# Kernel optimization log

Measured on AMD Instinct MI355X. Metric: run time of the kernel, lower is better.

Reference implementation:

```python
import jax, jax.numpy as jnp
import numpy as np

B, S, D, H = 2, 2048, 1024, 16
HD = D // H
FF = 4 * D
EPS = 1e-5


def _layernorm(x, g, b):
    m = jnp.mean(x, axis=-1, keepdims=True)
    v = jnp.var(x, axis=-1, keepdims=True)
    return (x - m) * jax.lax.rsqrt(v + EPS) * g + b


def setup_inputs() -> dict:
    key = jax.random.key(0)
    ks = jax.random.split(key, 13)
    s = lambda fan_in: 1.0 / np.sqrt(fan_in)
    return {
        "x": jax.random.normal(ks[0], (B, S, D), jnp.float32),
        "ln1_g": jnp.ones((D,), jnp.float32),
        "ln1_b": jnp.zeros((D,), jnp.float32),
        "w_qkv": jax.random.uniform(ks[1], (D, 3 * D), jnp.float32, -s(D), s(D)),
        "b_qkv": jax.random.uniform(ks[2], (3 * D,), jnp.float32, -s(D), s(D)),
        "w_proj": jax.random.uniform(ks[3], (D, D), jnp.float32, -s(D), s(D)),
        "b_proj": jax.random.uniform(ks[4], (D,), jnp.float32, -s(D), s(D)),
        "ln2_g": jnp.ones((D,), jnp.float32),
        "ln2_b": jnp.zeros((D,), jnp.float32),
        "w_fc1": jax.random.uniform(ks[5], (D, FF), jnp.float32, -s(D), s(D)),
        "b_fc1": jax.random.uniform(ks[6], (FF,), jnp.float32, -s(D), s(D)),
        "w_fc2": jax.random.uniform(ks[7], (FF, D), jnp.float32, -s(FF), s(FF)),
        "b_fc2": jax.random.uniform(ks[8], (D,), jnp.float32, -s(FF), s(FF)),
    }


def reference(x, ln1_g, ln1_b, w_qkv, b_qkv, w_proj, b_proj,
              ln2_g, ln2_b, w_fc1, b_fc1, w_fc2, b_fc2):
    scale = 1.0 / np.sqrt(HD)
    # pre-LN attention
    h = _layernorm(x, ln1_g, ln1_b)
    qkv = h @ w_qkv + b_qkv                                # [B,S,3D]
    qkv = qkv.reshape(B, S, 3, H, HD).transpose(2, 0, 3, 1, 4)
    q, k, v = qkv[0], qkv[1], qkv[2]                       # [B,H,S,HD]
    scores = jnp.einsum("bhqd,bhkd->bhqk", q, k) * scale   # [B,H,S,S]
    causal = jnp.tril(jnp.ones((S, S), bool))
    scores = jnp.where(causal, scores, -jnp.inf)
    attn = jax.nn.softmax(scores, axis=-1)
    out = jnp.einsum("bhqk,bhkd->bhqd", attn, v)           # [B,H,S,HD]
    out = out.transpose(0, 2, 1, 3).reshape(B, S, D)
    out = out @ w_proj + b_proj
    x = x + out
    # pre-LN MLP
    h = _layernorm(x, ln2_g, ln2_b)
    h = jax.nn.gelu(h @ w_fc1 + b_fc1, approximate=False)
    h = h @ w_fc2 + b_fc2
    return x + h
```

## Files before the change

### kernel.cpp

```cpp
#include <hip/hip_runtime.h>
#include <hip/hip_bf16.h>

#define BDIM 1024
#define SEQ  2048
#define NB   2
#define NH   16
#define HDIM 64
#define FFDIM 4096
#define MROWS (NB*SEQ)

typedef __attribute__((ext_vector_type(8))) short short8;
typedef __attribute__((ext_vector_type(4))) float f32x4;

static __device__ __forceinline__ unsigned short f2bf(float f) {
  union { float f; unsigned u; } v; v.f = f;
  unsigned r = v.u + 0x7fffu + ((v.u >> 16) & 1u);
  return (unsigned short)(r >> 16);
}

static __device__ __forceinline__ f32x4 splat4(float x) {
  f32x4 v; v[0] = x; v[1] = x; v[2] = x; v[3] = x; return v;
}

#define GLOAD16(gp, lp)                                                        \
  __builtin_amdgcn_global_load_lds(                                            \
      (const __attribute__((address_space(1))) void*)(gp),                     \
      (__attribute__((address_space(3))) void*)(lp), 16, 0, 0)

__global__ void tcvt_all(const float* __restrict__ w0, const float* __restrict__ w1,
                         const float* __restrict__ w2, const float* __restrict__ w3,
                         unsigned short* __restrict__ o0, unsigned short* __restrict__ o1,
                         unsigned short* __restrict__ o2, unsigned short* __restrict__ o3) {
  const int bid = blockIdx.x;
  const float* in; unsigned short* out; int R, C, nbx, rem;
  if (bid < 3072)      { in = w0; out = o0; R = 1024; C = 3072; rem = bid;        nbx = 96;  }
  else if (bid < 4096) { in = w1; out = o1; R = 1024; C = 1024; rem = bid - 3072; nbx = 32;  }
  else if (bid < 8192) { in = w2; out = o2; R = 1024; C = 4096; rem = bid - 4096; nbx = 128; }
  else                 { in = w3; out = o3; R = 4096; C = 1024; rem = bid - 8192; nbx = 32;  }
  const int c0 = (rem % nbx) * 32, r0 = (rem / nbx) * 32;
  __shared__ float tile[32][33];
  const int tx = threadIdx.x & 31, ty = threadIdx.x >> 5;
#pragma unroll
  for (int i = 0; i < 32; i += 8)
    tile[ty + i][tx] = in[(size_t)(r0 + ty + i) * C + c0 + tx];
  __syncthreads();
#pragma unroll
  for (int i = 0; i < 32; i += 8)
    out[(size_t)(c0 + ty + i) * R + r0 + tx] = f2bf(tile[tx][ty + i]);
}

__global__ void vtr_kernel(const unsigned short* __restrict__ qkv,
                           unsigned short* __restrict__ vt) {
  __shared__ unsigned short tile[32][33];
  const int h = blockIdx.z & 15, b = blockIdx.z >> 4;
  const int s0 = blockIdx.y * 32, d0 = blockIdx.x * 32;
  const int tx = threadIdx.x & 31, ty = threadIdx.x >> 5;
  const unsigned short* src = qkv + (size_t)b * SEQ * 3072 + 2048 + h * HDIM;
#pragma unroll
  for (int i = 0; i < 32; i += 8)
    tile[ty + i][tx] = src[(size_t)(s0 + ty + i) * 3072 + d0 + tx];
  __syncthreads();
  unsigned short* dst = vt + (size_t)(b * NH + h) * HDIM * SEQ;
#pragma unroll
  for (int i = 0; i < 32; i += 8)
    dst[(size_t)(d0 + ty + i) * SEQ + s0 + tx] = tile[tx][ty + i];
}

__global__ void ln_kernel(const float* __restrict__ x, const float* __restrict__ g,
                          const float* __restrict__ b, unsigned short* __restrict__ out) {
  const int row = blockIdx.x;
  const int tid = threadIdx.x;
  const float4 v = ((const float4*)(x + (size_t)row * BDIM))[tid];
  float s  = v.x + v.y + v.z + v.w;
  float ss = v.x * v.x + v.y * v.y + v.z * v.z + v.w * v.w;
#pragma unroll
  for (int off = 32; off; off >>= 1) { s += __shfl_xor(s, off); ss += __shfl_xor(ss, off); }
  __shared__ float red[8];
  const int wave = tid >> 6;
  if ((tid & 63) == 0) { red[wave * 2] = s; red[wave * 2 + 1] = ss; }
  __syncthreads();
  s  = red[0] + red[2] + red[4] + red[6];
  ss = red[1] + red[3] + red[5] + red[7];
  const float mean = s * (1.0f / BDIM);
  const float inv  = rsqrtf(ss * (1.0f / BDIM) - mean * mean + 1e-5f);
  const float4 gg = ((const float4*)g)[tid];
  const float4 bb = ((const float4*)b)[tid];
  ushort4 o;
  o.x = f2bf((v.x - mean) * inv * gg.x + bb.x);
  o.y = f2bf((v.y - mean) * inv * gg.y + bb.y);
  o.z = f2bf((v.z - mean) * inv * gg.z + bb.z);
  o.w = f2bf((v.w - mean) * inv * gg.w + bb.w);
  ((ushort4*)(out + (size_t)row * BDIM))[tid] = o;
}

template <int EPI>
__global__ __launch_bounds__(256, 2)
void gemm_bt(const unsigned short* __restrict__ A, const unsigned short* __restrict__ Bt,
             const float* __restrict__ bias, const float* __restrict__ resid,
             void* __restrict__ outp, int M, int N, int K) {
  __shared__ unsigned short As[128 * 32];
  __shared__ unsigned short Bs[128 * 32];
  const int tid = threadIdx.x;
  const int n0 = blockIdx.x * 128, m0 = blockIdx.y * 128;
  const int lane = tid & 63, wave = tid >> 6;
  const int lr = lane & 15, lg = lane >> 4;
  const int wr = (wave >> 1) * 64, wc = (wave & 1) * 64;

  const unsigned short* ga0 = A  + (size_t)(m0 + (tid >> 2)) * K + (tid & 3) * 8;
  const unsigned short* ga1 = ga0 + (size_t)64 * K;
  const unsigned short* gb0 = Bt + (size_t)(n0 + (tid >> 2)) * K + (tid & 3) * 8;
  const unsigned short* gb1 = gb0 + (size_t)64 * K;
  unsigned short* la0 = As + tid * 8;
  unsigned short* la1 = As + (256 + tid) * 8;
  unsigned short* lb0 = Bs + tid * 8;
  unsigned short* lb1 = Bs + (256 + tid) * 8;

  f32x4 acc[4][4];
#pragma unroll
  for (int i = 0; i < 4; i++)
#pragma unroll
    for (int j = 0; j < 4; j++) acc[i][j] = splat4(0.0f);

  for (int k0 = 0; k0 < K; k0 += 32) {
    GLOAD16(ga0 + k0, la0);
    GLOAD16(ga1 + k0, la1);
    GLOAD16(gb0 + k0, lb0);
    GLOAD16(gb1 + k0, lb1);
    __syncthreads();
    short8 af[4], bfr[4];
#pragma unroll
    for (int mi = 0; mi < 4; mi++)
      af[mi] = *(const short8*)(As + (wr + mi * 16 + lr) * 32 + lg * 8);
#pragma unroll
    for (int ni = 0; ni < 4; ni++)
      bfr[ni] = *(const short8*)(Bs + (wc + ni * 16 + lr) * 32 + lg * 8);
#pragma unroll
    for (int mi = 0; mi < 4; mi++)
#pragma unroll
      for (int ni = 0; ni < 4; ni++)
        acc[mi][ni] = __builtin_amdgcn_mfma_f32_16x16x32_bf16(af[mi], bfr[ni], acc[mi][ni], 0, 0, 0);
    __syncthreads();
  }

  float bv[4];
#pragma unroll
  for (int ni = 0; ni < 4; ni++) bv[ni] = bias[n0 + wc + ni * 16 + lr];
#pragma unroll
  for (int mi = 0; mi < 4; mi++) {
#pragma unroll
    for (int ni = 0; ni < 4; ni++) {
      const int row0 = m0 + wr + mi * 16 + lg * 4;
      const int col  = n0 + wc + ni * 16 + lr;
#pragma unroll
      for (int r = 0; r < 4; r++) {
        const float v = acc[mi][ni][r] + bv[ni];
        const size_t idx = (size_t)(row0 + r) * N + col;
        if constexpr (EPI == 0) {
          ((unsigned short*)outp)[idx] = f2bf(v);
        } else if constexpr (EPI == 1) {
          ((float*)outp)[idx] = v + resid[idx];
        } else {
          const float t = 0.5f * v * (1.0f + erff(v * 0.70710678118f));
          ((unsigned short*)outp)[idx] = f2bf(t);
        }
      }
    }
  }
}

__global__ __launch_bounds__(256, 3)
void attn_kernel(const unsigned short* __restrict__ qkv,
                 const unsigned short* __restrict__ vT,
                 unsigned short* __restrict__ out) {
  __shared__ unsigned short Ks[64 * 64];
  __shared__ unsigned short Vs[64 * 64];
  __shared__ unsigned short Ps[4][32 * 72];
  const int tid = threadIdx.x;
  const int wave = tid >> 6, lane = tid & 63;
  const int lr = lane & 15, lg = lane >> 4;
  const int Q0 = blockIdx.x * 128;
  const int wq0 = Q0 + wave * 32;
  const int h = blockIdx.y, bb = blockIdx.z;
  const size_t base = (size_t)bb * SEQ * 3072;
  const unsigned short* vth = vT + (size_t)(bb * NH + h) * HDIM * SEQ;
  unsigned short* psw = Ps[wave];
  const int sw = lr & 7;

  short8 qf[2][2];
#pragma unroll
  for (int qb = 0; qb < 2; ++qb)
#pragma unroll
    for (int kc = 0; kc < 2; ++kc)
      qf[qb][kc] = *(const short8*)(qkv + base +
          (size_t)(wq0 + qb * 16 + lr) * 3072 + h * HDIM + kc * 32 + lg * 8);

  f32x4 oacc[2][4];
#pragma unroll
  for (int qb = 0; qb < 2; ++qb)
#pragma unroll
    for (int n = 0; n < 4; ++n) oacc[qb][n] = splat4(0.0f);
  f32x4 m_i[2] = { splat4(-INFINITY), splat4(-INFINITY) };
  f32x4 l_i[2] = { splat4(0.0f), splat4(0.0f) };

  const int srow = tid >> 3;
  const int scb  = (tid & 7) ^ (srow & 7);
  const unsigned short* kg0 = qkv + base + (size_t)srow * 3072 + 1024 + h * HDIM + scb * 8;
  const unsigned short* vg0 = vth + (size_t)srow * SEQ + scb * 8;
  unsigned short* kl0 = Ks + tid * 8;
  unsigned short* kl1 = Ks + 2048 + tid * 8;
  unsigned short* vl0 = Vs + tid * 8;
  unsigned short* vl1 = Vs + 2048 + tid * 8;

  const int TB = Q0 / 64 + 2;

  for (int t = 0; t < TB; ++t) {
    const int kk = t * 64;
    __syncthreads();
    GLOAD16(kg0 + (size_t)kk * 3072, kl0);
    GLOAD16(kg0 + (size_t)(kk + 32) * 3072, kl1);
    GLOAD16(vg0 + kk, vl0);
    GLOAD16(vg0 + (size_t)32 * SEQ + kk, vl1);
    __syncthreads();

    short8 kf[4][2];
#pragma unroll
    for (int kb = 0; kb < 4; ++kb)
#pragma unroll
      for (int kc = 0; kc < 2; ++kc)
        kf[kb][kc] = *(const short8*)(Ks + (kb * 16 + lr) * 64 +
                                      (((kc * 4 + lg) ^ sw) * 8));
    f32x4 s[2][4];
#pragma unroll
    for (int qb = 0; qb < 2; ++qb)
#pragma unroll
      for (int kb = 0; kb < 4; ++kb) s[qb][kb] = splat4(0.0f);
    __builtin_amdgcn_s_setprio(1);
#pragma unroll
    for (int qb = 0; qb < 2; ++qb)
#pragma unroll
      for (int kb = 0; kb < 4; ++kb) {
        s[qb][kb] = __builtin_amdgcn_mfma_f32_16x16x32_bf16(qf[qb][0], kf[kb][0], s[qb][kb], 0, 0, 0);
        s[qb][kb] = __builtin_amdgcn_mfma_f32_16x16x32_bf16(qf[qb][1], kf[kb][1], s[qb][kb], 0, 0, 0);
      }
    __builtin_amdgcn_s_setprio(0);

    const bool nm = (kk + 64 > wq0);
#pragma unroll
    for (int qb = 0; qb < 2; ++qb)
#pragma unroll
      for (int kb = 0; kb < 4; ++kb)
#pragma unroll
        for (int r = 0; r < 4; ++r) {
          float v = s[qb][kb][r] * 0.125f;
          if (nm) {
            const int q = wq0 + qb * 16 + lg * 4 + r;
            if (kk + kb * 16 + lr > q) v = -INFINITY;
          }
          s[qb][kb][r] = v;
        }

    f32x4 mx[2];
#pragma unroll
    for (int qb = 0; qb < 2; ++qb) {
#pragma unroll
      for (int r = 0; r < 4; ++r)
        mx[qb][r] = fmaxf(fmaxf(s[qb][0][r], s[qb][1][r]),
                          fmaxf(s[qb][2][r], s[qb][3][r]));
    }
#pragma unroll
    for (int msk = 1; msk < 16; msk <<= 1)
#pragma unroll
      for (int qb = 0; qb < 2; ++qb)
#pragma unroll
        for (int r = 0; r < 4; ++r)
          mx[qb][r] = fmaxf(mx[qb][r], __shfl_xor(mx[qb][r], msk));
    f32x4 mnew[2], corr[2];
#pragma unroll
    for (int qb = 0; qb < 2; ++qb)
#pragma unroll
      for (int r = 0; r < 4; ++r) {
        mnew[qb][r] = fmaxf(m_i[qb][r], mx[qb][r]);
        corr[qb][r] = __expf(m_i[qb][r] - mnew[qb][r]);
      }
#pragma unroll
    for (int qb = 0; qb < 2; ++qb)
#pragma unroll
      for (int kb = 0; kb < 4; ++kb)
#pragma unroll
        for (int r = 0; r < 4; ++r)
          s[qb][kb][r] = __expf(s[qb][kb][r] - mnew[qb][r]);
    f32x4 ps[2];
#pragma unroll
    for (int qb = 0; qb < 2; ++qb)
#pragma unroll
      for (int r = 0; r < 4; ++r)
        ps[qb][r] = (s[qb][0][r] + s[qb][1][r]) + (s[qb][2][r] + s[qb][3][r]);
#pragma unroll
    for (int msk = 1; msk < 16; msk <<= 1)
#pragma unroll
      for (int qb = 0; qb < 2; ++qb)
#pragma unroll
        for (int r = 0; r < 4; ++r)
          ps[qb][r] += __shfl_xor(ps[qb][r], msk);
#pragma unroll
    for (int qb = 0; qb < 2; ++qb)
#pragma unroll
      for (int r = 0; r < 4; ++r) {
        l_i[qb][r] = l_i[qb][r] * corr[qb][r] + ps[qb][r];
        m_i[qb][r] = mnew[qb][r];
      }
#pragma unroll
    for (int qb = 0; qb < 2; ++qb)
#pragma unroll
      for (int n = 0; n < 4; ++n)
#pragma unroll
        for (int r = 0; r < 4; ++r) oacc[qb][n][r] *= corr[qb][r];

#pragma unroll
    for (int qb = 0; qb < 2; ++qb)
#pragma unroll
      for (int kb = 0; kb < 4; ++kb)
#pragma unroll
        for (int r = 0; r < 4; ++r)
          psw[(qb * 16 + lg * 4 + r) * 72 + kb * 16 + lr] = f2bf(s[qb][kb][r]);

    short8 pf[2][2], vf[4][2];
#pragma unroll
    for (int qb = 0; qb < 2; ++qb)
#pragma unroll
      for (int kc = 0; kc < 2; ++kc)
        pf[qb][kc] = *(const short8*)(psw + (qb * 16 + lr) * 72 + kc * 32 + lg * 8);
#pragma unroll
    for (int n = 0; n < 4; ++n)
#pragma unroll
      for (int kc = 0; kc < 2; ++kc)
        vf[n][kc] = *(const short8*)(Vs + (n * 16 + lr) * 64 +
                                     (((kc * 4 + lg) ^ sw) * 8));
    __builtin_amdgcn_s_setprio(1);
#pragma unroll
    for (int qb = 0; qb < 2; ++qb)
#pragma unroll
      for (int n = 0; n < 4; ++n) {
        oacc[qb][n] = __builtin_amdgcn_mfma_f32_16x16x32_bf16(pf[qb][0], vf[n][0], oacc[qb][n], 0, 0, 0);
        oacc[qb][n] = __builtin_amdgcn_mfma_f32_16x16x32_bf16(pf[qb][1], vf[n][1], oacc[qb][n], 0, 0, 0);
      }
    __builtin_amdgcn_s_setprio(0);
  }

  f32x4 linv[2];
#pragma unroll
  for (int qb = 0; qb < 2; ++qb)
#pragma unroll
    for (int r = 0; r < 4; ++r) linv[qb][r] = 1.0f / l_i[qb][r];
#pragma unroll
  for (int qb = 0; qb < 2; ++qb)
#pragma unroll
    for (int n = 0; n < 4; ++n)
#pragma unroll
      for (int r = 0; r < 4; ++r)
        out[(size_t)(bb * SEQ + wq0 + qb * 16 + lg * 4 + r) * BDIM + h * HDIM + n * 16 + lr]
            = f2bf(oacc[qb][n][r] * linv[qb][r]);
}

extern "C" void kernel_launch(void* const* d_in, const int* in_sizes, int n_in,
                              void* d_out, int out_size, void* d_ws, size_t ws_size,
                              hipStream_t stream) {
  const float* x      = (const float*)d_in[0];
  const float* ln1_g  = (const float*)d_in[1];
  const float* ln1_b  = (const float*)d_in[2];
  const float* w_qkv  = (const float*)d_in[3];
  const float* b_qkv  = (const float*)d_in[4];
  const float* w_proj = (const float*)d_in[5];
  const float* b_proj = (const float*)d_in[6];
  const float* ln2_g  = (const float*)d_in[7];
  const float* ln2_b  = (const float*)d_in[8];
  const float* w_fc1  = (const float*)d_in[9];
  const float* b_fc1  = (const float*)d_in[10];
  const float* w_fc2  = (const float*)d_in[11];
  const float* b_fc2  = (const float*)d_in[12];
  float* out = (float*)d_out;

  char* ws = (char*)d_ws;
  unsigned short* wqkvT  = (unsigned short*)(ws + 0);
  unsigned short* wprojT = (unsigned short*)(ws + 6291456);
  unsigned short* wfc1T  = (unsigned short*)(ws + 8388608);
  unsigned short* wfc2T  = (unsigned short*)(ws + 16777216);
  unsigned short* hbuf   = (unsigned short*)(ws + 25165824);
  float*          x2     = (float*)         (ws + 33554432);
  unsigned short* qkvb   = (unsigned short*)(ws + 50331648);
  unsigned short* attnb  = (unsigned short*)(ws + 75497472);
  unsigned short* fc1b   = (unsigned short*)(ws + 50331648);

  tcvt_all<<<12288, 256, 0, stream>>>(w_qkv, w_proj, w_fc1, w_fc2,
                                      wqkvT, wprojT, wfc1T, wfc2T);

  ln_kernel<<<MROWS, 256, 0, stream>>>(x, ln1_g, ln1_b, hbuf);
  gemm_bt<0><<<dim3(3072 / 128, MROWS / 128), 256, 0, stream>>>(hbuf, wqkvT, b_qkv, nullptr, qkvb, MROWS, 3072, 1024);
  vtr_kernel<<<dim3(HDIM / 32, SEQ / 32, NB * NH), 256, 0, stream>>>(qkvb, hbuf);
  attn_kernel<<<dim3(SEQ / 128, NH, NB), 256, 0, stream>>>(qkvb, hbuf, attnb);
  gemm_bt<1><<<dim3(1024 / 128, MROWS / 128), 256, 0, stream>>>(attnb, wprojT, b_proj, x, x2, MROWS, 1024, 1024);

  ln_kernel<<<MROWS, 256, 0, stream>>>(x2, ln2_g, ln2_b, hbuf);
  gemm_bt<2><<<dim3(4096 / 128, MROWS / 128), 256, 0, stream>>>(hbuf, wfc1T, b_fc1, nullptr, fc1b, MROWS, FFDIM, 1024);
  gemm_bt<1><<<dim3(1024 / 128, MROWS / 128), 256, 0, stream>>>(fc1b, wfc2T, b_fc2, x2, out, MROWS, 1024, FFDIM);
}
```

Baseline: 443.9 us.

## Vectorize transposes, shrink attention blocks, add N64 GEMM for narrow outputs

Vectorizes the weight-cast and V-transpose kernels with float4/short8 accesses. Attention becomes one 64-thread wave per 32-query block. It reads K/V fragments straight from global memory instead of staging them in LDS, uses exp2 with a pre-scaled log2e factor, and trims the causal loop bound per wave. A new 128x64-tile GEMM is used for the proj and fc2 outputs (N=1024) to launch more blocks, and the main GEMM's launch bounds go from 2 to 3 waves. Fine-grained causal work balance and better occupancy are traded for uncached, uncoalesced global fragment loads in attention.

```diff
diff --git a/kernel.cpp b/kernel.cpp
--- a/kernel.cpp
+++ b/kernel.cpp
@@ -38,32 +38,44 @@
   else if (bid < 8192) { in = w2; out = o2; R = 1024; C = 4096; rem = bid - 4096; nbx = 128; }
   else                 { in = w3; out = o3; R = 4096; C = 1024; rem = bid - 8192; nbx = 32;  }
   const int c0 = (rem % nbx) * 32, r0 = (rem / nbx) * 32;
-  __shared__ float tile[32][33];
-  const int tx = threadIdx.x & 31, ty = threadIdx.x >> 5;
-#pragma unroll
-  for (int i = 0; i < 32; i += 8)
-    tile[ty + i][tx] = in[(size_t)(r0 + ty + i) * C + c0 + tx];
+  __shared__ float tile[32][36];
+  const int t = threadIdx.x;
+  {
+    const int row = t >> 3, col4 = (t & 7) * 4;
+    const float4 v = *(const float4*)(in + (size_t)(r0 + row) * C + c0 + col4);
+    *(float4*)&tile[row][col4] = v;
+  }
   __syncthreads();
-#pragma unroll
-  for (int i = 0; i < 32; i += 8)
-    out[(size_t)(c0 + ty + i) * R + r0 + tx] = f2bf(tile[tx][ty + i]);
+  {
+    const int c = t & 31, rg = t >> 5;
+    ushort4 o;
+    o.x = f2bf(tile[rg * 4 + 0][c]);
+    o.y = f2bf(tile[rg * 4 + 1][c]);
+    o.z = f2bf(tile[rg * 4 + 2][c]);
+    o.w = f2bf(tile[rg * 4 + 3][c]);
+    *(ushort4*)(out + (size_t)(c0 + c) * R + r0 + rg * 4) = o;
+  }
 }
 
 __global__ void vtr_kernel(const unsigned short* __restrict__ qkv,
                            unsigned short* __restrict__ vt) {
-  __shared__ unsigned short tile[32][33];
+  __shared__ unsigned short tile[32][72];
   const int h = blockIdx.z & 15, b = blockIdx.z >> 4;
-  const int s0 = blockIdx.y * 32, d0 = blockIdx.x * 32;
-  const int tx = threadIdx.x & 31, ty = threadIdx.x >> 5;
-  const unsigned short* src = qkv + (size_t)b * SEQ * 3072 + 2048 + h * HDIM;
-#pragma unroll
-  for (int i = 0; i < 32; i += 8)
-    tile[ty + i][tx] = src[(size_t)(s0 + ty + i) * 3072 + d0 + tx];
+  const int s0 = blockIdx.y * 64, d0 = blockIdx.x * 32;
+  const int t = threadIdx.x;
+  const unsigned short* src = qkv + (size_t)b * SEQ * 3072 + 2048 + h * HDIM + d0;
+  {
+    const int s = t & 63, d8 = (t >> 6) * 8;
+    const short8 v = *(const short8*)(src + (size_t)(s0 + s) * 3072 + d8);
+#pragma unroll
+    for (int j = 0; j < 8; ++j) tile[d8 + j][s] = (unsigned short)v[j];
+  }
   __syncthreads();
-  unsigned short* dst = vt + (size_t)(b * NH + h) * HDIM * SEQ;
-#pragma unroll
-  for (int i = 0; i < 32; i += 8)
-    dst[(size_t)(d0 + ty + i) * SEQ + s0 + tx] = tile[tx][ty + i];
+  {
+    const int d = t >> 3, s8 = (t & 7) * 8;
+    const short8 v = *(const short8*)&tile[d][s8];
+    *(short8*)(vt + (size_t)(b * NH + h) * HDIM * SEQ + (size_t)(d0 + d) * SEQ + s0 + s8) = v;
+  }
 }
 
 __global__ void ln_kernel(const float* __restrict__ x, const float* __restrict__ g,
@@ -94,7 +106,7 @@
 }
 
 template <int EPI>
-__global__ __launch_bounds__(256, 2)
+__global__ __launch_bounds__(256, 3)
 void gemm_bt(const unsigned short* __restrict__ A, const unsigned short* __restrict__ Bt,
              const float* __restrict__ bias, const float* __restrict__ resid,
              void* __restrict__ outp, int M, int N, int K) {
@@ -169,22 +181,81 @@
 }
 
 __global__ __launch_bounds__(256, 3)
+void gemm_bt_n64(const unsigned short* __restrict__ A, const unsigned short* __restrict__ Bt,
+                 const float* __restrict__ bias, const float* __restrict__ resid,
+                 float* __restrict__ outp, int M, int N, int K) {
+  __shared__ unsigned short As[128 * 32];
+  __shared__ unsigned short Bs[64 * 32];
+  const int tid = threadIdx.x;
+  const int n0 = blockIdx.x * 64, m0 = blockIdx.y * 128;
+  const int lane = tid & 63, wave = tid >> 6;
+  const int lr = lane & 15, lg = lane >> 4;
+  const int wr = wave * 32;
+
+  const unsigned short* ga0 = A  + (size_t)(m0 + (tid >> 2)) * K + (tid & 3) * 8;
+  const unsigned short* ga1 = ga0 + (size_t)64 * K;
+  const unsigned short* gb0 = Bt + (size_t)(n0 + (tid >> 2)) * K + (tid & 3) * 8;
+  unsigned short* la0 = As + tid * 8;
+  unsigned short* la1 = As + (256 + tid) * 8;
+  unsigned short* lb0 = Bs + tid * 8;
+
+  f32x4 acc[2][4];
+#pragma unroll
+  for (int i = 0; i < 2; i++)
+#pragma unroll
+    for (int j = 0; j < 4; j++) acc[i][j] = splat4(0.0f);
+
+  for (int k0 = 0; k0 < K; k0 += 32) {
+    GLOAD16(ga0 + k0, la0);
+    GLOAD16(ga1 + k0, la1);
+    GLOAD16(gb0 + k0, lb0);
+    __syncthreads();
+    short8 af[2], bfr[4];
+#pragma unroll
+    for (int mi = 0; mi < 2; mi++)
+      af[mi] = *(const short8*)(As + (wr + mi * 16 + lr) * 32 + lg * 8);
+#pragma unroll
+    for (int ni = 0; ni < 4; ni++)
+      bfr[ni] = *(const short8*)(Bs + (ni * 16 + lr) * 32 + lg * 8);
+#pragma unroll
+    for (int mi = 0; mi < 2; mi++)
+#pragma unroll
+      for (int ni = 0; ni < 4; ni++)
+        acc[mi][ni] = __builtin_amdgcn_mfma_f32_16x16x32_bf16(af[mi], bfr[ni], acc[mi][ni], 0, 0, 0);
+    __syncthreads();
+  }
+
+  float bv[4];
+#pragma unroll
+  for (int ni = 0; ni < 4; ni++) bv[ni] = bias[n0 + ni * 16 + lr];
+#pragma unroll
+  for (int mi = 0; mi < 2; mi++) {
+#pragma unroll
+    for (int ni = 0; ni < 4; ni++) {
+      const int row0 = m0 + wr + mi * 16 + lg * 4;
+      const int col  = n0 + ni * 16 + lr;
+#pragma unroll
+      for (int r = 0; r < 4; r++) {
+        const size_t idx = (size_t)(row0 + r) * N + col;
+        outp[idx] = acc[mi][ni][r] + bv[ni] + resid[idx];
+      }
+    }
+  }
+}
+
+__global__ __launch_bounds__(64, 3)
 void attn_kernel(const unsigned short* __restrict__ qkv,
                  const unsigned short* __restrict__ vT,
                  unsigned short* __restrict__ out) {
-  __shared__ unsigned short Ks[64 * 64];
-  __shared__ unsigned short Vs[64 * 64];
-  __shared__ unsigned short Ps[4][32 * 72];
-  const int tid = threadIdx.x;
-  const int wave = tid >> 6, lane = tid & 63;
+  __shared__ unsigned short psw[32 * 72];
+  const int lane = threadIdx.x & 63;
   const int lr = lane & 15, lg = lane >> 4;
-  const int Q0 = blockIdx.x * 128;
-  const int wq0 = Q0 + wave * 32;
+  const int wq0 = blockIdx.x * 32;
   const int h = blockIdx.y, bb = blockIdx.z;
   const size_t base = (size_t)bb * SEQ * 3072;
+  const unsigned short* kb_g = qkv + base + 1024 + h * HDIM;
   const unsigned short* vth = vT + (size_t)(bb * NH + h) * HDIM * SEQ;
-  unsigned short* psw = Ps[wave];
-  const int sw = lr & 7;
+  const float SC = 0.125f * 1.44269504089f;
 
   short8 qf[2][2];
 #pragma unroll
@@ -202,33 +273,17 @@
   f32x4 m_i[2] = { splat4(-INFINITY), splat4(-INFINITY) };
   f32x4 l_i[2] = { splat4(0.0f), splat4(0.0f) };
 
-  const int srow = tid >> 3;
-  const int scb  = (tid & 7) ^ (srow & 7);
-  const unsigned short* kg0 = qkv + base + (size_t)srow * 3072 + 1024 + h * HDIM + scb * 8;
-  const unsigned short* vg0 = vth + (size_t)srow * SEQ + scb * 8;
-  unsigned short* kl0 = Ks + tid * 8;
-  unsigned short* kl1 = Ks + 2048 + tid * 8;
-  unsigned short* vl0 = Vs + tid * 8;
-  unsigned short* vl1 = Vs + 2048 + tid * 8;
-
-  const int TB = Q0 / 64 + 2;
+  const int TB = wq0 / 64 + 1;
 
   for (int t = 0; t < TB; ++t) {
     const int kk = t * 64;
-    __syncthreads();
-    GLOAD16(kg0 + (size_t)kk * 3072, kl0);
-    GLOAD16(kg0 + (size_t)(kk + 32) * 3072, kl1);
-    GLOAD16(vg0 + kk, vl0);
-    GLOAD16(vg0 + (size_t)32 * SEQ + kk, vl1);
-    __syncthreads();
-
     short8 kf[4][2];
 #pragma unroll
     for (int kb = 0; kb < 4; ++kb)
 #pragma unroll
       for (int kc = 0; kc < 2; ++kc)
-        kf[kb][kc] = *(const short8*)(Ks + (kb * 16 + lr) * 64 +
-                                      (((kc * 4 + lg) ^ sw) * 8));
+        kf[kb][kc] = *(const short8*)(kb_g + (size_t)(kk + kb * 16 + lr) * 3072 +
+                                      kc * 32 + lg * 8);
     f32x4 s[2][4];
 #pragma unroll
     for (int qb = 0; qb < 2; ++qb)
@@ -251,7 +306,7 @@
       for (int kb = 0; kb < 4; ++kb)
 #pragma unroll
         for (int r = 0; r < 4; ++r) {
-          float v = s[qb][kb][r] * 0.125f;
+          float v = s[qb][kb][r] * SC;
           if (nm) {
             const int q = wq0 + qb * 16 + lg * 4 + r;
             if (kk + kb * 16 + lr > q) v = -INFINITY;
@@ -261,12 +316,11 @@
 
     f32x4 mx[2];
 #pragma unroll
-    for (int qb = 0; qb < 2; ++qb) {
+    for (int qb = 0; qb < 2; ++qb)
 #pragma unroll
       for (int r = 0; r < 4; ++r)
         mx[qb][r] = fmaxf(fmaxf(s[qb][0][r], s[qb][1][r]),
                           fmaxf(s[qb][2][r], s[qb][3][r]));
-    }
 #pragma unroll
     for (int msk = 1; msk < 16; msk <<= 1)
 #pragma unroll
@@ -280,7 +334,7 @@
 #pragma unroll
       for (int r = 0; r < 4; ++r) {
         mnew[qb][r] = fmaxf(m_i[qb][r], mx[qb][r]);
-        corr[qb][r] = __expf(m_i[qb][r] - mnew[qb][r]);
+        corr[qb][r] = exp2f(m_i[qb][r] - mnew[qb][r]);
       }
 #pragma unroll
     for (int qb = 0; qb < 2; ++qb)
@@ -288,7 +342,7 @@
       for (int kb = 0; kb < 4; ++kb)
 #pragma unroll
         for (int r = 0; r < 4; ++r)
-          s[qb][kb][r] = __expf(s[qb][kb][r] - mnew[qb][r]);
+          s[qb][kb][r] = exp2f(s[qb][kb][r] - mnew[qb][r]);
     f32x4 ps[2];
 #pragma unroll
     for (int qb = 0; qb < 2; ++qb)
@@ -334,8 +388,8 @@
     for (int n = 0; n < 4; ++n)
 #pragma unroll
       for (int kc = 0; kc < 2; ++kc)
-        vf[n][kc] = *(const short8*)(Vs + (n * 16 + lr) * 64 +
-                                     (((kc * 4 + lg) ^ sw) * 8));
+        vf[n][kc] = *(const short8*)(vth + (size_t)(n * 16 + lr) * SEQ +
+                                     kk + kc * 32 + lg * 8);
     __builtin_amdgcn_s_setprio(1);
 #pragma unroll
     for (int qb = 0; qb < 2; ++qb)
@@ -396,11 +450,11 @@
 
   ln_kernel<<<MROWS, 256, 0, stream>>>(x, ln1_g, ln1_b, hbuf);
   gemm_bt<0><<<dim3(3072 / 128, MROWS / 128), 256, 0, stream>>>(hbuf, wqkvT, b_qkv, nullptr, qkvb, MROWS, 3072, 1024);
-  vtr_kernel<<<dim3(HDIM / 32, SEQ / 32, NB * NH), 256, 0, stream>>>(qkvb, hbuf);
-  attn_kernel<<<dim3(SEQ / 128, NH, NB), 256, 0, stream>>>(qkvb, hbuf, attnb);
-  gemm_bt<1><<<dim3(1024 / 128, MROWS / 128), 256, 0, stream>>>(attnb, wprojT, b_proj, x, x2, MROWS, 1024, 1024);
+  vtr_kernel<<<dim3(HDIM / 32, SEQ / 64, NB * NH), 256, 0, stream>>>(qkvb, hbuf);
+  attn_kernel<<<dim3(SEQ / 32, NH, NB), 64, 0, stream>>>(qkvb, hbuf, attnb);
+  gemm_bt_n64<<<dim3(1024 / 64, MROWS / 128), 256, 0, stream>>>(attnb, wprojT, b_proj, x, x2, MROWS, 1024, 1024);
 
   ln_kernel<<<MROWS, 256, 0, stream>>>(x2, ln2_g, ln2_b, hbuf);
   gemm_bt<2><<<dim3(4096 / 128, MROWS / 128), 256, 0, stream>>>(hbuf, wfc1T, b_fc1, nullptr, fc1b, MROWS, FFDIM, 1024);
-  gemm_bt<1><<<dim3(1024 / 128, MROWS / 128), 256, 0, stream>>>(fc1b, wfc2T, b_fc2, x2, out, MROWS, 1024, FFDIM);
-}
+  gemm_bt_n64<<<dim3(1024 / 64, MROWS / 128), 256, 0, stream>>>(fc1b, wfc2T, b_fc2, x2, out, MROWS, 1024, FFDIM);
+}
```

After: 465.5 us. 4.9% more time.
